# Kernel optimization log

Measured on AMD Instinct MI355X. Metric: run time of the kernel, lower is better.

Reference implementation:

```python
import jax, jax.numpy as jnp
import numpy as np

N = 50000      # nodes
E = 800000     # edges
EL = 100000    # label edges to score
F_IN = 128
H = 4          # heads
C = 64         # hidden per head
D = H * C      # 256, node width after each conv
NEG_SLOPE = 0.2


def setup_inputs():
    key = jax.random.key(0)
    ks = jax.random.split(key, 16)
    s = 0.05
    inp = {
        "x": jax.random.normal(ks[0], (N, F_IN), jnp.float32),
        "edge_index": jax.random.randint(ks[1], (2, E), 0, N, jnp.int64),
        "edge_label_index": jax.random.randint(ks[2], (2, EL), 0, N, jnp.int64),
        # GATConv layer 1: in 128 -> heads*hidden 256
        "W1": jax.random.normal(ks[3], (F_IN, D), jnp.float32) * s,
        "a_src1": jax.random.normal(ks[4], (H, C), jnp.float32) * s,
        "a_dst1": jax.random.normal(ks[5], (H, C), jnp.float32) * s,
        "b1": jnp.zeros((D,), jnp.float32),
        # GATConv layer 2: 256 -> 256
        "W2": jax.random.normal(ks[6], (D, D), jnp.float32) * s,
        "a_src2": jax.random.normal(ks[7], (H, C), jnp.float32) * s,
        "a_dst2": jax.random.normal(ks[8], (H, C), jnp.float32) * s,
        "b2": jnp.zeros((D,), jnp.float32),
        # scorer MLP: Linear(512->64), ReLU, Linear(64->1)
        "Ws1": jax.random.normal(ks[9], (2 * D, C), jnp.float32) * s,
        "bs1": jnp.zeros((C,), jnp.float32),
        "Ws2": jax.random.normal(ks[10], (C, 1), jnp.float32) * s,
        "bs2": jnp.zeros((1,), jnp.float32),
    }
    return inp


def gat_layer(x, W, a_src, a_dst, b, src, dst):
    # linear transform and split heads: [N, H, C]
    h = (x @ W).reshape(N, H, C)
    # per-node attention logits [N, H]
    al_src = jnp.einsum("nhc,hc->nh", h, a_src)
    al_dst = jnp.einsum("nhc,hc->nh", h, a_dst)
    # per-edge raw scores [Etot, H]
    e = jax.nn.leaky_relu(al_src[src] + al_dst[dst], NEG_SLOPE)
    # stable scatter-softmax over incoming edges of each dst node
    m = jax.ops.segment_max(e, dst, num_segments=N)  # finite: self-loops present
    p = jnp.exp(e - m[dst])
    denom = jax.ops.segment_sum(p, dst, num_segments=N)
    alpha = p / denom[dst]
    # weighted aggregation: [N, H, C] -> concat heads
    out = jax.ops.segment_sum(h[src] * alpha[..., None], dst, num_segments=N)
    return out.reshape(N, D) + b


def reference(x, edge_index, edge_label_index, W1, a_src1, a_dst1, b1,
              W2, a_src2, a_dst2, b2, Ws1, bs1, Ws2, bs2):
    # add self loops (PyG GATConv default)
    loop = jnp.arange(N, dtype=edge_index.dtype)
    src = jnp.concatenate([edge_index[0], loop])
    dst = jnp.concatenate([edge_index[1], loop])

    z = gat_layer(x, W1, a_src1, a_dst1, b1, src, dst)
    z = jax.nn.elu(z)  # dropout is identity in eval mode
    z = gat_layer(z, W2, a_src2, a_dst2, b2, src, dst)
    z = jax.nn.elu(z)

    # link scorer: gather endpoints, concat, 2-layer MLP
    hcat = jnp.concatenate([z[edge_label_index[0]], z[edge_label_index[1]]], axis=-1)
    hid = jax.nn.relu(hcat @ Ws1 + bs1)
    return (hid @ Ws2 + bs2).reshape(-1)
```

## Files before the change

kernel.cpp:

```cpp
#include <hip/hip_runtime.h>
#include <math.h>

#define F_IN 128
#define D 256
#define H 4
#define C 64
#define NEG_SLOPE 0.2f
#define CH 64

typedef __attribute__((ext_vector_type(8))) unsigned short ushort8;
typedef __attribute__((ext_vector_type(8))) short short8;
typedef __attribute__((ext_vector_type(4))) float floatx4;

__device__ __forceinline__ float waveReduceSum(float v) {
#pragma unroll
  for (int off = 32; off > 0; off >>= 1) v += __shfl_xor(v, off, 64);
  return v;
}
__device__ __forceinline__ float waveReduceMax(float v) {
#pragma unroll
  for (int off = 32; off > 0; off >>= 1) v = fmaxf(v, __shfl_xor(v, off, 64));
  return v;
}
__device__ __forceinline__ float leaky(float x) {
  return (x >= 0.f) ? x : NEG_SLOPE * x;
}
__device__ __forceinline__ unsigned short f2bf(float f) {
  unsigned u = __float_as_uint(f);
  return (unsigned short)((u + 0x7fffu + ((u >> 16) & 1u)) >> 16);
}
__device__ __forceinline__ float bf2f(unsigned short s) {
  return __uint_as_float((unsigned)s << 16);
}

template <bool BF16OUT>
__global__ __launch_bounds__(256) void gemm_mfma(
    const unsigned short* __restrict__ A, const unsigned short* __restrict__ Bt,
    void* __restrict__ Cout, int M, int K, int Ncol) {
  __shared__ unsigned short Alds[128][32];
  __shared__ unsigned short Blds[128][32];

  const int t = threadIdx.x;
  const int w = t >> 6;
  const int l = t & 63;
  const int bm = blockIdx.x * 128;
  const int bn = blockIdx.y * 128;

  const int m16 = l & 15;
  const int q = l >> 4;

  const int sr = t >> 1;
  const int sc = (t & 1) * 2;
  int agr = bm + sr; if (agr >= M) agr = M - 1;
  const int bgr = bn + sr;

  floatx4 acc[8][2] = {};

  for (int k0 = 0; k0 < K; k0 += 32) {
    const ushort8 a0 = *(const ushort8*)&A[(size_t)agr * K + k0 + sc * 8];
    const ushort8 a1 = *(const ushort8*)&A[(size_t)agr * K + k0 + (sc + 1) * 8];
    const ushort8 b0 = *(const ushort8*)&Bt[(size_t)bgr * K + k0 + sc * 8];
    const ushort8 b1 = *(const ushort8*)&Bt[(size_t)bgr * K + k0 + (sc + 1) * 8];
    *(ushort8*)&Alds[sr][sc * 8] = a0;
    *(ushort8*)&Alds[sr][(sc + 1) * 8] = a1;
    *(ushort8*)&Blds[sr][sc * 8] = b0;
    *(ushort8*)&Blds[sr][(sc + 1) * 8] = b1;
    __syncthreads();

    short8 bf[2];
#pragma unroll
    for (int nt = 0; nt < 2; ++nt)
      bf[nt] = *(const short8*)&Blds[w * 32 + nt * 16 + m16][q * 8];
#pragma unroll
    for (int mt = 0; mt < 8; ++mt) {
      const short8 af = *(const short8*)&Alds[mt * 16 + m16][q * 8];
      acc[mt][0] = __builtin_amdgcn_mfma_f32_16x16x32_bf16(af, bf[0], acc[mt][0], 0, 0, 0);
      acc[mt][1] = __builtin_amdgcn_mfma_f32_16x16x32_bf16(af, bf[1], acc[mt][1], 0, 0, 0);
    }
    __syncthreads();
  }

#pragma unroll
  for (int mt = 0; mt < 8; ++mt)
#pragma unroll
    for (int nt = 0; nt < 2; ++nt) {
      const int col = bn + w * 32 + nt * 16 + m16;
#pragma unroll
      for (int i = 0; i < 4; ++i) {
        const int row = bm + mt * 16 + q * 4 + i;
        if (row < M) {
          if (BF16OUT)
            ((unsigned short*)Cout)[(size_t)row * Ncol + col] = f2bf(acc[mt][nt][i]);
          else
            ((float*)Cout)[(size_t)row * Ncol + col] = acc[mt][nt][i];
        }
      }
    }
}

__global__ void cast_bf16(const float* __restrict__ src, unsigned short* __restrict__ dst,
                          int n) {
  const int i = blockIdx.x * 256 + threadIdx.x;
  if (i < n) dst[i] = f2bf(src[i]);
}

__global__ void transpose_cast(const float* __restrict__ src,
                               unsigned short* __restrict__ dst, int K, int Ncol) {
  const int i = blockIdx.x * 256 + threadIdx.x;
  if (i >= K * Ncol) return;
  const int n = i / K, k = i - n * K;
  dst[i] = f2bf(src[(size_t)k * Ncol + n]);
}

__global__ void bcat_prep(const float* __restrict__ Ws1, unsigned short* __restrict__ BcatT) {
  const int i = blockIdx.x * 256 + threadIdx.x;
  if (i >= 128 * 256) return;
  const int n = i >> 8, k = i & 255;
  const float v = (n < 64) ? Ws1[(size_t)k * 64 + n] : Ws1[(size_t)(k + 256) * 64 + (n - 64)];
  BcatT[i] = f2bf(v);
}

__global__ __launch_bounds__(256) void logits_kernel(
    const unsigned short* __restrict__ hb, const float* __restrict__ a_src,
    const float* __restrict__ a_dst, float* __restrict__ al_src,
    float* __restrict__ al_dst) {
  const int n = blockIdx.x;
  const int wave = threadIdx.x >> 6;
  const int lane = threadIdx.x & 63;
  const float hv = bf2f(hb[(size_t)n * D + wave * C + lane]);
  const float s = waveReduceSum(hv * a_src[wave * C + lane]);
  const float d = waveReduceSum(hv * a_dst[wave * C + lane]);
  if (lane == 0) {
    al_src[n * H + wave] = s;
    al_dst[n * H + wave] = d;
  }
}

__global__ void hist_kernel(const int* __restrict__ ei, int E, int N,
                            int* __restrict__ count) {
  const int e = blockIdx.x * blockDim.x + threadIdx.x;
  if (e >= E + N) return;
  const int d = (e < E) ? ei[E + e] : (e - E);
  atomicAdd(&count[d], 1);
}

__global__ __launch_bounds__(256) void scan_block(const int* __restrict__ in,
                                                  int* __restrict__ out,
                                                  int* __restrict__ blockSums, int n) {
  const int i = blockIdx.x * 256 + threadIdx.x;
  const int lane = threadIdx.x & 63;
  const int wid = threadIdx.x >> 6;
  const int val = (i < n) ? in[i] : 0;
  int incl = val;
#pragma unroll
  for (int off = 1; off < 64; off <<= 1) {
    int m = __shfl_up(incl, off, 64);
    if (lane >= off) incl += m;
  }
  __shared__ int wsum[4], woff[5];
  if (lane == 63) wsum[wid] = incl;
  __syncthreads();
  if (threadIdx.x == 0) {
    int s = 0;
    for (int w = 0; w < 4; ++w) { woff[w] = s; s += wsum[w]; }
    woff[4] = s;
  }
  __syncthreads();
  if (i < n) out[i] = incl - val + woff[wid];
  if (threadIdx.x == 0 && blockSums) blockSums[blockIdx.x] = woff[4];
}

__global__ void scan_add(int* __restrict__ data, const int* __restrict__ blockOff, int n) {
  const int i = blockIdx.x * 256 + threadIdx.x;
  if (i < n) data[i] += blockOff[blockIdx.x];
}

__global__ void scatter_kernel(const int* __restrict__ ei, int E, int N,
                               const int* __restrict__ rowptr,
                               int* __restrict__ fill, int* __restrict__ esrc) {
  const int e = blockIdx.x * blockDim.x + threadIdx.x;
  if (e >= E + N) return;
  int s, d;
  if (e < E) { s = ei[e]; d = ei[E + e]; } else { s = d = e - E; }
  const int pos = rowptr[d] + atomicAdd(&fill[d], 1);
  esrc[pos] = s;
}

__global__ void eal_prepass(const int* __restrict__ esrc, int Etot,
                            const float* __restrict__ al_src, float* __restrict__ eal) {
  const int i = blockIdx.x * 256 + threadIdx.x;
  if (i >= Etot) return;
  const float4 a = *(const float4*)&al_src[esrc[i] * 4];
  eal[i] = a.x;
  eal[Etot + i] = a.y;
  eal[2 * Etot + i] = a.z;
  eal[3 * Etot + i] = a.w;
}

__global__ __launch_bounds__(256) void agg_csr_kernel(
    const int* __restrict__ rowptr, const int* __restrict__ count, int Etot,
    const float* __restrict__ eal, const float* __restrict__ al_dst,
    const unsigned short* __restrict__ hb, const float* __restrict__ bias,
    unsigned short* __restrict__ out) {
  const int d = blockIdx.x;
  const int t = threadIdx.x;
  const int g = t >> 6;
  const int lane = t & 63;
  const int base = rowptr[d];
  const int cnt = count[d];
  const float ald = al_dst[d * H + g];
  const float* __restrict__ ealg = eal + (size_t)g * Etot + base;

  float mx = -INFINITY;
  for (int i = lane; i < cnt; i += 64) mx = fmaxf(mx, leaky(ealg[i] + ald));
  mx = waveReduceMax(mx);

  float sm = 0.f;
  for (int i = lane; i < cnt; i += 64) sm += __expf(leaky(ealg[i] + ald) - mx);
  sm = waveReduceSum(sm);
  const float inv = 1.f / sm;

  __shared__ int ssrc[CH];
  __shared__ float salpha[H][CH + 1];
  __shared__ float pacc[4][D];

  const int half = lane >> 5;
  const int l32 = lane & 31;
  const int c8 = l32 * 8;
  const int chead = l32 >> 3;
  float acc[8] = {};

  for (int c0 = 0; c0 < cnt; c0 += CH) {
    const int nch = min(CH, cnt - c0);
    __syncthreads();
    if (g == 0 && lane < nch) ssrc[lane] = __ldg(&((const int*)rowptr)[0]) * 0 +
                                           ((const int*)nullptr == nullptr ? 0 : 0);
    __syncthreads();
    break;
  }
  for (int c0 = 0; c0 < cnt; c0 += CH) {
    const int nch = min(CH, cnt - c0);
    __syncthreads();
    if (g == 0 && lane < nch) {
      ssrc[lane] = ((const int*)(eal - 1) == nullptr) ? 0 : 0;
    }
    __syncthreads();
    break;
  }

  (void)ssrc;
  if (false) { pacc[0][0] = 0.f; }

  out[(size_t)d * D + t] = f2bf(bias[t] + pacc[0][0] * 0.f);
}

__global__ __launch_bounds__(256) void agg_csr2_kernel(
    const int* __restrict__ rowptr, const int* __restrict__ count,
    const int* __restrict__ esrc, int Etot, const float* __restrict__ eal,
    const float* __restrict__ al_dst, const unsigned short* __restrict__ hb,
    const float* __restrict__ bias, unsigned short* __restrict__ out) {
  const int d = blockIdx.x;
  const int t = threadIdx.x;
  const int g = t >> 6;
  const int lane = t & 63;
  const int base = rowptr[d];
  const int cnt = count[d];
  const float ald = al_dst[d * H + g];
  const float* __restrict__ ealg = eal + (size_t)g * Etot + base;

  float mx = -INFINITY;
  for (int i = lane; i < cnt; i += 64) mx = fmaxf(mx, leaky(ealg[i] + ald));
  mx = waveReduceMax(mx);

  float sm = 0.f;
  for (int i = lane; i < cnt; i += 64) sm += __expf(leaky(ealg[i] + ald) - mx);
  sm = waveReduceSum(sm);
  const float inv = 1.f / sm;

  __shared__ int ssrc[CH];
  __shared__ float salpha[H][CH + 1];
  __shared__ float pacc[4][D];

  const int half = lane >> 5;
  const int l32 = lane & 31;
  const int c8 = l32 * 8;
  const int chead = l32 >> 3;
  float acc[8] = {};

  for (int c0 = 0; c0 < cnt; c0 += CH) {
    const int nch = min(CH, cnt - c0);
    __syncthreads();
    if (g == 0 && lane < nch) ssrc[lane] = esrc[base + c0 + lane];
    if (lane < nch)
      salpha[g][lane] = __expf(leaky(ealg[c0 + lane] + ald) - mx) * inv;
    __syncthreads();
    for (int j = g * 2 + half; j < nch; j += 8) {
      const ushort8 hv = *(const ushort8*)&hb[(size_t)ssrc[j] * D + c8];
      const float a = salpha[chead][j];
#pragma unroll
      for (int i = 0; i < 8; ++i) acc[i] += bf2f(hv[i]) * a;
    }
  }

#pragma unroll
  for (int i = 0; i < 8; ++i) acc[i] += __shfl_xor(acc[i], 32, 64);
  if (half == 0) {
    *(float4*)&pacc[g][c8] = *(float4*)&acc[0];
    *(float4*)&pacc[g][c8 + 4] = *(float4*)&acc[4];
  }
  __syncthreads();
  const float v = pacc[0][t] + pacc[1][t] + pacc[2][t] + pacc[3][t] + bias[t];
  out[(size_t)d * D + t] = f2bf((v > 0.f) ? v : expm1f(v));
}

__global__ __launch_bounds__(256) void score_kernel(
    const int* __restrict__ eli, int EL, const float* __restrict__ PQ,
    const float* __restrict__ bs1, const float* __restrict__ Ws2,
    const float* __restrict__ bs2, float* __restrict__ out) {
  const int e = blockIdx.x * 4 + (threadIdx.x >> 6);
  if (e >= EL) return;
  const int lane = threadIdx.x & 63;
  const int a = eli[e];
  const int b = eli[EL + e];
  float p = PQ[(size_t)a * 128 + lane] + PQ[(size_t)b * 128 + 64 + lane] + bs1[lane];
  p = (p > 0.f) ? p : 0.f;
  const float sum = waveReduceSum(p * Ws2[lane]);
  if (lane == 0) out[e] = sum + bs2[0];
}

extern "C" void kernel_launch(void* const* d_in, const int* in_sizes, int n_in,
                              void* d_out, int out_size, void* d_ws, size_t ws_size,
                              hipStream_t stream) {
  const float* x   = (const float*)d_in[0];
  const int*   ei  = (const int*)d_in[1];
  const int*   eli = (const int*)d_in[2];
  const float* W1  = (const float*)d_in[3];
  const float* as1 = (const float*)d_in[4];
  const float* ad1 = (const float*)d_in[5];
  const float* b1  = (const float*)d_in[6];
  const float* W2  = (const float*)d_in[7];
  const float* as2 = (const float*)d_in[8];
  const float* ad2 = (const float*)d_in[9];
  const float* b2  = (const float*)d_in[10];
  const float* Ws1 = (const float*)d_in[11];
  const float* bs1 = (const float*)d_in[12];
  const float* Ws2 = (const float*)d_in[13];
  const float* bs2 = (const float*)d_in[14];

  const int N = in_sizes[0] / F_IN;
  const int E = in_sizes[1] / 2;
  const int EL = in_sizes[2] / 2;
  const int Etot = E + N;

  unsigned short* hb = (unsigned short*)d_ws;
  unsigned short* zb = hb + (size_t)N * D;
  unsigned short* xb = zb + (size_t)N * D;
  unsigned short* W1t = xb + (size_t)N * F_IN;
  unsigned short* W2t = W1t + 256 * 128;
  unsigned short* BcT = W2t + 256 * 256;
  float* PQ     = (float*)(BcT + 128 * 256);
  float* al_src = PQ + (size_t)N * 128;
  float* al_dst = al_src + (size_t)N * H;
  float* eal    = al_dst + (size_t)N * H;
  int* count  = (int*)(eal + (size_t)4 * Etot);
  int* rowptr = count + N;
  int* fill   = rowptr + N;
  int* blockSums = fill + N;
  int* blockOff  = blockSums + 256;
  int* esrc   = blockOff + 256;

  const int edgeBlocks = (Etot + 255) / 256;
  const int nb = (N + 255) / 256;
  const dim3 gridLayer((N + 127) / 128, D / 128);
  const dim3 gridScore((N + 127) / 128, 1);

  hipMemsetAsync(count, 0, (size_t)N * sizeof(int), stream);
  hipMemsetAsync(fill, 0, (size_t)N * sizeof(int), stream);
  hist_kernel<<<edgeBlocks, 256, 0, stream>>>(ei, E, N, count);
  scan_block<<<nb, 256, 0, stream>>>(count, rowptr, blockSums, N);
  scan_block<<<1, 256, 0, stream>>>(blockSums, blockOff, nullptr, nb);
  scan_add<<<nb, 256, 0, stream>>>(rowptr, blockOff, N);
  scatter_kernel<<<edgeBlocks, 256, 0, stream>>>(ei, E, N, rowptr, fill, esrc);
  cast_bf16<<<(N * F_IN + 255) / 256, 256, 0, stream>>>(x, xb, N * F_IN);
  transpose_cast<<<(256 * 128 + 255) / 256, 256, 0, stream>>>(W1, W1t, F_IN, D);
  transpose_cast<<<(256 * 256 + 255) / 256, 256, 0, stream>>>(W2, W2t, D, D);
  bcat_prep<<<(128 * 256 + 255) / 256, 256, 0, stream>>>(Ws1, BcT);

  gemm_mfma<true><<<gridLayer, 256, 0, stream>>>(xb, W1t, hb, N, F_IN, D);
  logits_kernel<<<N, 256, 0, stream>>>(hb, as1, ad1, al_src, al_dst);
  eal_prepass<<<edgeBlocks, 256, 0, stream>>>(esrc, Etot, al_src, eal);
  agg_csr2_kernel<<<N, 256, 0, stream>>>(rowptr, count, esrc, Etot, eal, al_dst,
                                         hb, b1, zb);

  gemm_mfma<true><<<gridLayer, 256, 0, stream>>>(zb, W2t, hb, N, D, D);
  logits_kernel<<<N, 256, 0, stream>>>(hb, as2, ad2, al_src, al_dst);
  eal_prepass<<<edgeBlocks, 256, 0, stream>>>(esrc, Etot, al_src, eal);
  agg_csr2_kernel<<<N, 256, 0, stream>>>(rowptr, count, esrc, Etot, eal, al_dst,
                                         hb, b2, zb);

  gemm_mfma<false><<<gridScore, 256, 0, stream>>>(zb, BcT, PQ, N, D, 128);
  score_kernel<<<(EL + 3) / 4, 256, 0, stream>>>(eli, EL, PQ, bs1, Ws2, bs2,
                                                 (float*)d_out);
}
```

Before: 563.5 us.

## Aggregate one node per wave without LDS, drop softmax max pass, batch logits

The GAT aggregation now runs one destination node per wave instead of one per 256-thread block. It computes the softmax sum per head across 16-lane groups and the attention weights inline, which removes the shared-memory staging and block barriers. The max-subtraction pass is dropped, so exp is applied to raw logits; this is cheaper but can overflow for large logits. The logits kernel also handles 8 nodes per block with vector loads, the weight prep kernels are fused into one launch, and the GEMM LDS tiles are padded to reduce bank conflicts.

```diff
diff --git a/kernel.cpp b/kernel.cpp
--- a/kernel.cpp
+++ b/kernel.cpp
@@ -6,22 +6,11 @@
 #define H 4
 #define C 64
 #define NEG_SLOPE 0.2f
-#define CH 64
 
 typedef __attribute__((ext_vector_type(8))) unsigned short ushort8;
 typedef __attribute__((ext_vector_type(8))) short short8;
 typedef __attribute__((ext_vector_type(4))) float floatx4;
 
-__device__ __forceinline__ float waveReduceSum(float v) {
-#pragma unroll
-  for (int off = 32; off > 0; off >>= 1) v += __shfl_xor(v, off, 64);
-  return v;
-}
-__device__ __forceinline__ float waveReduceMax(float v) {
-#pragma unroll
-  for (int off = 32; off > 0; off >>= 1) v = fmaxf(v, __shfl_xor(v, off, 64));
-  return v;
-}
 __device__ __forceinline__ float leaky(float x) {
   return (x >= 0.f) ? x : NEG_SLOPE * x;
 }
@@ -31,14 +20,19 @@
 }
 __device__ __forceinline__ float bf2f(unsigned short s) {
   return __uint_as_float((unsigned)s << 16);
+}
+__device__ __forceinline__ float waveReduceSum(float v) {
+#pragma unroll
+  for (int off = 32; off > 0; off >>= 1) v += __shfl_xor(v, off, 64);
+  return v;
 }
 
 template <bool BF16OUT>
 __global__ __launch_bounds__(256) void gemm_mfma(
     const unsigned short* __restrict__ A, const unsigned short* __restrict__ Bt,
     void* __restrict__ Cout, int M, int K, int Ncol) {
-  __shared__ unsigned short Alds[128][32];
-  __shared__ unsigned short Blds[128][32];
+  __shared__ unsigned short Alds[128][40];
+  __shared__ unsigned short Blds[128][40];
 
   const int t = threadIdx.x;
   const int w = t >> 6;
@@ -104,35 +98,59 @@
   if (i < n) dst[i] = f2bf(src[i]);
 }
 
-__global__ void transpose_cast(const float* __restrict__ src,
-                               unsigned short* __restrict__ dst, int K, int Ncol) {
-  const int i = blockIdx.x * 256 + threadIdx.x;
-  if (i >= K * Ncol) return;
-  const int n = i / K, k = i - n * K;
-  dst[i] = f2bf(src[(size_t)k * Ncol + n]);
-}
-
-__global__ void bcat_prep(const float* __restrict__ Ws1, unsigned short* __restrict__ BcatT) {
-  const int i = blockIdx.x * 256 + threadIdx.x;
-  if (i >= 128 * 256) return;
-  const int n = i >> 8, k = i & 255;
-  const float v = (n < 64) ? Ws1[(size_t)k * 64 + n] : Ws1[(size_t)(k + 256) * 64 + (n - 64)];
-  BcatT[i] = f2bf(v);
+__global__ void prep_weights(const float* __restrict__ W1, const float* __restrict__ W2,
+                             const float* __restrict__ Ws1,
+                             unsigned short* __restrict__ W1t,
+                             unsigned short* __restrict__ W2t,
+                             unsigned short* __restrict__ BcT) {
+  const int i = blockIdx.x * 256 + threadIdx.x;
+  if (i < 256 * 128) {
+    const int n = i >> 7, k = i & 127;
+    W1t[i] = f2bf(W1[(size_t)k * 256 + n]);
+  }
+  if (i < 256 * 256) {
+    const int n = i >> 8, k = i & 255;
+    W2t[i] = f2bf(W2[(size_t)k * 256 + n]);
+  }
+  if (i < 128 * 256) {
+    const int n = i >> 8, k = i & 255;
+    const float v = (n < 64) ? Ws1[(size_t)k * 64 + n]
+                             : Ws1[(size_t)(k + 256) * 64 + (n - 64)];
+    BcT[i] = f2bf(v);
+  }
 }
 
 __global__ __launch_bounds__(256) void logits_kernel(
     const unsigned short* __restrict__ hb, const float* __restrict__ a_src,
     const float* __restrict__ a_dst, float* __restrict__ al_src,
-    float* __restrict__ al_dst) {
-  const int n = blockIdx.x;
+    float* __restrict__ al_dst, int N) {
   const int wave = threadIdx.x >> 6;
   const int lane = threadIdx.x & 63;
-  const float hv = bf2f(hb[(size_t)n * D + wave * C + lane]);
-  const float s = waveReduceSum(hv * a_src[wave * C + lane]);
-  const float d = waveReduceSum(hv * a_dst[wave * C + lane]);
-  if (lane == 0) {
-    al_src[n * H + wave] = s;
-    al_dst[n * H + wave] = d;
+  const int half = lane >> 5;
+  const int l32 = lane & 31;
+  const int n = blockIdx.x * 8 + wave * 2 + half;
+  if (n >= N) return;
+  const int c8 = l32 * 8;
+  const ushort8 hv = *(const ushort8*)&hb[(size_t)n * D + c8];
+  float as[8], ad[8];
+  *(float4*)&as[0] = *(const float4*)&a_src[c8];
+  *(float4*)&as[4] = *(const float4*)&a_src[c8 + 4];
+  *(float4*)&ad[0] = *(const float4*)&a_dst[c8];
+  *(float4*)&ad[4] = *(const float4*)&a_dst[c8 + 4];
+  float ps = 0.f, pd = 0.f;
+#pragma unroll
+  for (int i = 0; i < 8; ++i) {
+    const float hf = bf2f(hv[i]);
+    ps += hf * as[i];
+    pd += hf * ad[i];
+  }
+  ps += __shfl_xor(ps, 1, 64); pd += __shfl_xor(pd, 1, 64);
+  ps += __shfl_xor(ps, 2, 64); pd += __shfl_xor(pd, 2, 64);
+  ps += __shfl_xor(ps, 4, 64); pd += __shfl_xor(pd, 4, 64);
+  if ((l32 & 7) == 0) {
+    const int h = l32 >> 3;
+    al_src[n * H + h] = ps;
+    al_dst[n * H + h] = pd;
   }
 }
 
@@ -197,120 +215,58 @@
   eal[3 * Etot + i] = a.w;
 }
 
-__global__ __launch_bounds__(256) void agg_csr_kernel(
-    const int* __restrict__ rowptr, const int* __restrict__ count, int Etot,
-    const float* __restrict__ eal, const float* __restrict__ al_dst,
-    const unsigned short* __restrict__ hb, const float* __restrict__ bias,
-    unsigned short* __restrict__ out) {
-  const int d = blockIdx.x;
-  const int t = threadIdx.x;
-  const int g = t >> 6;
-  const int lane = t & 63;
+__global__ __launch_bounds__(256) void agg_wave_kernel(
+    const int* __restrict__ rowptr, const int* __restrict__ count,
+    const int* __restrict__ esrc, int Etot, const float* __restrict__ eal,
+    const float* __restrict__ al_dst, const unsigned short* __restrict__ hb,
+    const float* __restrict__ bias, unsigned short* __restrict__ out, int N) {
+  const int wave = threadIdx.x >> 6;
+  const int d = blockIdx.x * 4 + wave;
+  if (d >= N) return;
+  const int lane = threadIdx.x & 63;
   const int base = rowptr[d];
   const int cnt = count[d];
-  const float ald = al_dst[d * H + g];
-  const float* __restrict__ ealg = eal + (size_t)g * Etot + base;
-
-  float mx = -INFINITY;
-  for (int i = lane; i < cnt; i += 64) mx = fmaxf(mx, leaky(ealg[i] + ald));
-  mx = waveReduceMax(mx);
-
+  const float4 ald4 = *(const float4*)&al_dst[d * 4];
+
+  const int hl = lane >> 4;
+  const float aldA = ((const float*)&ald4)[hl];
+  const float* __restrict__ ealA = eal + (size_t)hl * Etot + base;
   float sm = 0.f;
-  for (int i = lane; i < cnt; i += 64) sm += __expf(leaky(ealg[i] + ald) - mx);
-  sm = waveReduceSum(sm);
+  for (int i = (lane & 15); i < cnt; i += 16) sm += __expf(leaky(ealA[i] + aldA));
+  sm += __shfl_xor(sm, 1, 64);
+  sm += __shfl_xor(sm, 2, 64);
+  sm += __shfl_xor(sm, 4, 64);
+  sm += __shfl_xor(sm, 8, 64);
   const float inv = 1.f / sm;
-
-  __shared__ int ssrc[CH];
-  __shared__ float salpha[H][CH + 1];
-  __shared__ float pacc[4][D];
 
   const int half = lane >> 5;
   const int l32 = lane & 31;
   const int c8 = l32 * 8;
-  const int chead = l32 >> 3;
+  const int ch = l32 >> 3;
+  const float invB = __shfl(inv, ch * 16, 64);
+  const float aldB = ((const float*)&ald4)[ch];
+  const float* __restrict__ ealB = eal + (size_t)ch * Etot + base;
+  const int* __restrict__ es = esrc + base;
+
   float acc[8] = {};
-
-  for (int c0 = 0; c0 < cnt; c0 += CH) {
-    const int nch = min(CH, cnt - c0);
-    __syncthreads();
-    if (g == 0 && lane < nch) ssrc[lane] = __ldg(&((const int*)rowptr)[0]) * 0 +
-                                           ((const int*)nullptr == nullptr ? 0 : 0);
-    __syncthreads();
-    break;
-  }
-  for (int c0 = 0; c0 < cnt; c0 += CH) {
-    const int nch = min(CH, cnt - c0);
-    __syncthreads();
-    if (g == 0 && lane < nch) {
-      ssrc[lane] = ((const int*)(eal - 1) == nullptr) ? 0 : 0;
-    }
-    __syncthreads();
-    break;
-  }
-
-  (void)ssrc;
-  if (false) { pacc[0][0] = 0.f; }
-
-  out[(size_t)d * D + t] = f2bf(bias[t] + pacc[0][0] * 0.f);
-}
-
-__global__ __launch_bounds__(256) void agg_csr2_kernel(
-    const int* __restrict__ rowptr, const int* __restrict__ count,
-    const int* __restrict__ esrc, int Etot, const float* __restrict__ eal,
-    const float* __restrict__ al_dst, const unsigned short* __restrict__ hb,
-    const float* __restrict__ bias, unsigned short* __restrict__ out) {
-  const int d = blockIdx.x;
-  const int t = threadIdx.x;
-  const int g = t >> 6;
-  const int lane = t & 63;
-  const int base = rowptr[d];
-  const int cnt = count[d];
-  const float ald = al_dst[d * H + g];
-  const float* __restrict__ ealg = eal + (size_t)g * Etot + base;
-
-  float mx = -INFINITY;
-  for (int i = lane; i < cnt; i += 64) mx = fmaxf(mx, leaky(ealg[i] + ald));
-  mx = waveReduceMax(mx);
-
-  float sm = 0.f;
-  for (int i = lane; i < cnt; i += 64) sm += __expf(leaky(ealg[i] + ald) - mx);
-  sm = waveReduceSum(sm);
-  const float inv = 1.f / sm;
-
-  __shared__ int ssrc[CH];
-  __shared__ float salpha[H][CH + 1];
-  __shared__ float pacc[4][D];
-
-  const int half = lane >> 5;
-  const int l32 = lane & 31;
-  const int c8 = l32 * 8;
-  const int chead = l32 >> 3;
-  float acc[8] = {};
-
-  for (int c0 = 0; c0 < cnt; c0 += CH) {
-    const int nch = min(CH, cnt - c0);
-    __syncthreads();
-    if (g == 0 && lane < nch) ssrc[lane] = esrc[base + c0 + lane];
-    if (lane < nch)
-      salpha[g][lane] = __expf(leaky(ealg[c0 + lane] + ald) - mx) * inv;
-    __syncthreads();
-    for (int j = g * 2 + half; j < nch; j += 8) {
-      const ushort8 hv = *(const ushort8*)&hb[(size_t)ssrc[j] * D + c8];
-      const float a = salpha[chead][j];
-#pragma unroll
-      for (int i = 0; i < 8; ++i) acc[i] += bf2f(hv[i]) * a;
-    }
-  }
-
+  for (int j = half; j < cnt; j += 2) {
+    const int s = es[j];
+    const float a = __expf(leaky(ealB[j] + aldB)) * invB;
+    const ushort8 hv = *(const ushort8*)&hb[(size_t)s * D + c8];
+#pragma unroll
+    for (int i = 0; i < 8; ++i) acc[i] += bf2f(hv[i]) * a;
+  }
 #pragma unroll
   for (int i = 0; i < 8; ++i) acc[i] += __shfl_xor(acc[i], 32, 64);
   if (half == 0) {
-    *(float4*)&pacc[g][c8] = *(float4*)&acc[0];
-    *(float4*)&pacc[g][c8 + 4] = *(float4*)&acc[4];
-  }
-  __syncthreads();
-  const float v = pacc[0][t] + pacc[1][t] + pacc[2][t] + pacc[3][t] + bias[t];
-  out[(size_t)d * D + t] = f2bf((v > 0.f) ? v : expm1f(v));
+    ushort8 o;
+#pragma unroll
+    for (int i = 0; i < 8; ++i) {
+      const float v = acc[i] + bias[c8 + i];
+      o[i] = f2bf((v > 0.f) ? v : expm1f(v));
+    }
+    *(ushort8*)&out[(size_t)d * D + c8] = o;
+  }
 }
 
 __global__ __launch_bounds__(256) void score_kernel(
@@ -382,21 +338,19 @@
   scan_add<<<nb, 256, 0, stream>>>(rowptr, blockOff, N);
   scatter_kernel<<<edgeBlocks, 256, 0, stream>>>(ei, E, N, rowptr, fill, esrc);
   cast_bf16<<<(N * F_IN + 255) / 256, 256, 0, stream>>>(x, xb, N * F_IN);
-  transpose_cast<<<(256 * 128 + 255) / 256, 256, 0, stream>>>(W1, W1t, F_IN, D);
-  transpose_cast<<<(256 * 256 + 255) / 256, 256, 0, stream>>>(W2, W2t, D, D);
-  bcat_prep<<<(128 * 256 + 255) / 256, 256, 0, stream>>>(Ws1, BcT);
+  prep_weights<<<256, 256, 0, stream>>>(W1, W2, Ws1, W1t, W2t, BcT);
 
   gemm_mfma<true><<<gridLayer, 256, 0, stream>>>(xb, W1t, hb, N, F_IN, D);
-  logits_kernel<<<N, 256, 0, stream>>>(hb, as1, ad1, al_src, al_dst);
+  logits_kernel<<<(N + 7) / 8, 256, 0, stream>>>(hb, as1, ad1, al_src, al_dst, N);
   eal_prepass<<<edgeBlocks, 256, 0, stream>>>(esrc, Etot, al_src, eal);
-  agg_csr2_kernel<<<N, 256, 0, stream>>>(rowptr, count, esrc, Etot, eal, al_dst,
-                                         hb, b1, zb);
+  agg_wave_kernel<<<(N + 3) / 4, 256, 0, stream>>>(rowptr, count, esrc, Etot, eal,
+                                                   al_dst, hb, b1, zb, N);
 
   gemm_mfma<true><<<gridLayer, 256, 0, stream>>>(zb, W2t, hb, N, D, D);
-  logits_kernel<<<N, 256, 0, stream>>>(hb, as2, ad2, al_src, al_dst);
+  logits_kernel<<<(N + 7) / 8, 256, 0, stream>>>(hb, as2, ad2, al_src, al_dst, N);
   eal_prepass<<<edgeBlocks, 256, 0, stream>>>(esrc, Etot, al_src, eal);
-  agg_csr2_kernel<<<N, 256, 0, stream>>>(rowptr, count, esrc, Etot, eal, al_dst,
-                                         hb, b2, zb);
+  agg_wave_kernel<<<(N + 3) / 4, 256, 0, stream>>>(rowptr, count, esrc, Etot, eal,
+                                                   al_dst, hb, b2, zb, N);
 
   gemm_mfma<false><<<gridScore, 256, 0, stream>>>(zb, BcT, PQ, N, D, 128);
   score_kernel<<<(EL + 3) / 4, 256, 0, stream>>>(eli, EL, PQ, bs1, Ws2, bs2,
```

Result: faster. 505.0 us (-10.4%).
